# Kernel tuning notes

Hardware: AMD Instinct MI355X
Metric: run time of the kernel (lower is better)

The kernel has to match this reference:

```python
import jax, jax.numpy as jnp
import numpy as np
from jax import lax
from jax.scipy.special import logsumexp

NUM_TAGS = 17
INPUT_DIM = 1024
B, S = 256, 512


def setup_inputs() -> dict:
    key = jax.random.key(0)
    ks = jax.random.split(key, 7)
    data = jax.random.normal(ks[0], (B, S, INPUT_DIM), dtype=jnp.float32)
    labels = jax.random.randint(ks[1], (B, S), 0, NUM_TAGS)
    mask = jnp.ones((B, S), dtype=bool)  # torchcrf requires mask[:,0] all True
    W = jax.random.normal(ks[2], (NUM_TAGS, INPUT_DIM), dtype=jnp.float32) / np.sqrt(INPUT_DIM)
    b = jnp.zeros((NUM_TAGS,), dtype=jnp.float32)
    # torchcrf initializes transition params ~ U(-0.1, 0.1)
    start_trans = jax.random.uniform(ks[3], (NUM_TAGS,), minval=-0.1, maxval=0.1)
    end_trans = jax.random.uniform(ks[4], (NUM_TAGS,), minval=-0.1, maxval=0.1)
    transitions = jax.random.uniform(ks[5], (NUM_TAGS, NUM_TAGS), minval=-0.1, maxval=0.1)
    return {"data": data, "labels": labels, "mask": mask, "W": W, "b": b,
            "start_trans": start_trans, "end_trans": end_trans, "transitions": transitions}


def _crf_nll(data, labels, mask, W, b, start_trans, end_trans, transitions):
    # emissions: [B, S, T]
    em = jnp.einsum('bsd,td->bst', data, W) + b
    # time-major views
    em_t = em.transpose(1, 0, 2)          # [S, B, T]
    tags = labels.T                        # [S, B]
    m = mask.T.astype(em.dtype)            # [S, B]
    bidx = jnp.arange(data.shape[0])

    # ---- numerator: score of the gold path ----
    score0 = start_trans[tags[0]] + em_t[0, bidx, tags[0]]  # [B]

    def num_step(score, inp):
        e_t, tag_prev, tag_t, m_t = inp
        score = score + (transitions[tag_prev, tag_t] + e_t[bidx, tag_t]) * m_t
        return score, None

    score, _ = lax.scan(num_step, score0, (em_t[1:], tags[:-1], tags[1:], m[1:]))
    last_idx = mask.sum(axis=1).astype(jnp.int32) - 1
    last_tags = labels[bidx, last_idx]
    score = score + end_trans[last_tags]

    # ---- denominator: forward algorithm (log partition) ----
    alpha0 = start_trans[None, :] + em_t[0]  # [B, T]

    def den_step(alpha, inp):
        e_t, m_t = inp
        # [B, Tprev, Tnext]
        nxt = logsumexp(alpha[:, :, None] + transitions[None, :, :] + e_t[:, None, :], axis=1)
        alpha = jnp.where(m_t[:, None] > 0, nxt, alpha)
        return alpha, None

    alpha, _ = lax.scan(den_step, alpha0, (em_t[1:], m[1:]))
    denom = logsumexp(alpha + end_trans[None, :], axis=1)  # [B]

    llh = score - denom
    return -llh.mean()  # reduction='mean', module returns -loglik


def reference(data, labels, mask, W, b, start_trans, end_trans, transitions):
    return _crf_nll(data, labels, mask, W, b, start_trans, end_trans, transitions)
```

## Files before the change

### kernel.cpp

```cpp
#include <hip/hip_runtime.h>
#include <hip/hip_bf16.h>


#define BB 256
#define SS 512
#define DD 1024
#define TT 17
#define ROWS (BB * SS)

typedef float f32x4 __attribute__((ext_vector_type(4)));
typedef short s16x8 __attribute__((ext_vector_type(8)));

__device__ inline unsigned bfr(unsigned u) { return (u + 0x7fffu + ((u >> 16) & 1u)) >> 16; }
__device__ inline unsigned pk2(float x, float y) {
    return bfr(__float_as_uint(x)) | (bfr(__float_as_uint(y)) << 16);
}

__device__ inline void lds_barrier() {
    __builtin_amdgcn_s_waitcnt(0xC00F);
    __builtin_amdgcn_s_barrier();
}

__device__ inline float bcast(float x, int l) {
    return __uint_as_float((unsigned)__builtin_amdgcn_readlane((int)__float_as_uint(x), l));
}

#define LDA 40

__global__ __launch_bounds__(256) void emis_kernel(
    const float* __restrict__ data, const float* __restrict__ W,
    const float* __restrict__ bias, float* __restrict__ em)
{
    __shared__ __align__(16) short At[256 * LDA];
    const int tid = threadIdx.x;
    const size_t row0 = (size_t)blockIdx.x * 256;
    const int wv = tid >> 6, ln = tid & 63;
    const int nl = ln & 15, quad = ln >> 4;
    const int c4 = tid & 7, rr = tid >> 3;
    const bool w1act = (nl == 0);

    const float* gbase  = data + (row0 + rr) * DD + c4 * 4;
    const float* w0base = W + nl * DD + quad * 8;
    const float* w1base = W + 16 * DD + quad * 8;

    float4 a[8];
    float4 wa, wb, va, vb;
    va = make_float4(0.f, 0.f, 0.f, 0.f); vb = va;

#pragma unroll
    for (int i = 0; i < 8; i++) a[i] = *(const float4*)(gbase + (size_t)i * 32 * DD);
    wa = *(const float4*)(w0base);
    wb = *(const float4*)(w0base + 4);
    if (w1act) { va = *(const float4*)(w1base); vb = *(const float4*)(w1base + 4); }

    f32x4 acc[4][2];
#pragma unroll
    for (int m = 0; m < 4; m++) {
        acc[m][0] = (f32x4){0.f, 0.f, 0.f, 0.f};
        acc[m][1] = (f32x4){0.f, 0.f, 0.f, 0.f};
    }

    for (int ks = 0; ks < 32; ks++) {
        if (ks) lds_barrier();
#pragma unroll
        for (int i = 0; i < 8; i++) {
            uint2 p; p.x = pk2(a[i].x, a[i].y); p.y = pk2(a[i].z, a[i].w);
            *(uint2*)(&At[(rr + 32 * i) * LDA + c4 * 4]) = p;
        }
        union { s16x8 v; unsigned u[4]; } b0u, b1u;
        b0u.u[0] = pk2(wa.x, wa.y); b0u.u[1] = pk2(wa.z, wa.w);
        b0u.u[2] = pk2(wb.x, wb.y); b0u.u[3] = pk2(wb.z, wb.w);
        b1u.u[0] = pk2(va.x, va.y); b1u.u[1] = pk2(va.z, va.w);
        b1u.u[2] = pk2(vb.x, vb.y); b1u.u[3] = pk2(vb.z, vb.w);
        if (ks < 31) {
            const float* gn = gbase + (ks + 1) * 32;
#pragma unroll
            for (int i = 0; i < 8; i++) a[i] = *(const float4*)(gn + (size_t)i * 32 * DD);
            const float* w0n = w0base + (ks + 1) * 32;
            wa = *(const float4*)(w0n); wb = *(const float4*)(w0n + 4);
            if (w1act) {
                const float* w1n = w1base + (ks + 1) * 32;
                va = *(const float4*)(w1n); vb = *(const float4*)(w1n + 4);
            }
        }
        lds_barrier();
#pragma unroll
        for (int mt = 0; mt < 4; mt++) {
            s16x8 af = *(s16x8*)(&At[(wv * 64 + mt * 16 + nl) * LDA + quad * 8]);
            acc[mt][0] = __builtin_amdgcn_mfma_f32_16x16x32_bf16(af, b0u.v, acc[mt][0], 0, 0, 0);
            acc[mt][1] = __builtin_amdgcn_mfma_f32_16x16x32_bf16(af, b1u.v, acc[mt][1], 0, 0, 0);
        }
    }

    const float bs0 = bias[nl];
    const float bs16 = bias[16];
#pragma unroll
    for (int mt = 0; mt < 4; mt++) {
        const size_t rbase = row0 + wv * 64 + mt * 16 + quad * 4;
#pragma unroll
        for (int r = 0; r < 4; r++) {
            em[(rbase + r) * TT + nl] = acc[mt][0][r] + bs0;
            if (w1act) em[(rbase + r) * TT + 16] = acc[mt][1][r] + bs16;
        }
    }
}

__global__ __launch_bounds__(64) void crf_scan_kernel(
    const float* __restrict__ em, const int* __restrict__ labels,
    const float* __restrict__ start_t, const float* __restrict__ end_t,
    const float* __restrict__ trans, float* __restrict__ res)
{
    const int b = blockIdx.x;
    const int lane = threadIdx.x;
    const float* em_b = em + (size_t)b * SS * TT;
    const int* lab = labels + b * SS;
    __shared__ float sE[64 * TT + TT];

    float part = 0.f;
    for (int t = lane; t < SS; t += 64) {
        const int tag = lab[t];
        float c = em_b[t * TT + tag];
        if (t == 0) c += start_t[tag];
        else        c += trans[lab[t - 1] * TT + tag];
        if (t == SS - 1) c += end_t[tag];
        part += c;
    }
#pragma unroll
    for (int off = 32; off; off >>= 1) part += __shfl_xor(part, off);
    const float score = part;

    const bool act = lane < TT;
    const int j = act ? lane : 0;
    float Tcol[TT];
#pragma unroll
    for (int i = 0; i < TT; i++) Tcol[i] = __expf(trans[i * TT + j]);

    float A = act ? __expf(start_t[j] + em_b[j]) : 0.f;
    float logZ = 0.f;

    for (int t0 = 0; t0 < SS; t0 += 64) {
        __syncthreads();
#pragma unroll
        for (int i = 0; i < TT; i++) {
            const int flat = i * 64 + lane;
            sE[flat] = __expf(em_b[t0 * TT + flat]);
        }
        __syncthreads();
        int dt = (t0 == 0) ? 1 : 0;
        float e = sE[dt * TT + j];
        for (; dt < 64; dt++) {
            const float en = sE[(dt + 1) * TT + j];
            float v0 = bcast(A, 0) * Tcol[0];
            float v1 = bcast(A, 1) * Tcol[1];
            float v2 = bcast(A, 2) * Tcol[2];
            float v3 = bcast(A, 3) * Tcol[3];
#pragma unroll
            for (int i = 4; i < 16; i += 4) {
                v0 = fmaf(bcast(A, i + 0), Tcol[i + 0], v0);
                v1 = fmaf(bcast(A, i + 1), Tcol[i + 1], v1);
                v2 = fmaf(bcast(A, i + 2), Tcol[i + 2], v2);
                v3 = fmaf(bcast(A, i + 3), Tcol[i + 3], v3);
            }
            v0 = fmaf(bcast(A, 16), Tcol[16], v0);
            A = ((v0 + v1) + (v2 + v3)) * e;
            if (((t0 + dt) & 3) == 3) {
                const float s = bcast(A, 0);
                const float r = __builtin_amdgcn_rcpf(s);
                logZ -= __logf(r);
                A *= r;
            }
            e = en;
        }
    }

    float fv = act ? A * __expf(end_t[j]) : 0.f;
#pragma unroll
    for (int off = 16; off; off >>= 1) fv += __shfl_xor(fv, off);
    const float denom = logZ + __logf(fv);

    if (lane == 0) res[b] = denom - score;
}

__global__ __launch_bounds__(256) void reduce_kernel(
    const float* __restrict__ res, float* __restrict__ out)
{
    const int tid = threadIdx.x;
    float v = res[tid];
#pragma unroll
    for (int off = 32; off; off >>= 1) v += __shfl_xor(v, off);
    __shared__ float ws[4];
    if ((tid & 63) == 0) ws[tid >> 6] = v;
    __syncthreads();
    if (tid == 0) out[0] = (ws[0] + ws[1] + ws[2] + ws[3]) * (1.0f / BB);
}

extern "C" void kernel_launch(void* const* d_in, const int* in_sizes, int n_in,
                              void* d_out, int out_size, void* d_ws, size_t ws_size,
                              hipStream_t stream) {
    const float* data   = (const float*)d_in[0];
    const int*   labels = (const int*)d_in[1];
    const float* W      = (const float*)d_in[3];
    const float* bias   = (const float*)d_in[4];
    const float* st     = (const float*)d_in[5];
    const float* en     = (const float*)d_in[6];
    const float* trans  = (const float*)d_in[7];

    float* em  = (float*)d_ws;
    float* res = (float*)((char*)d_ws + (size_t)ROWS * TT * 4);

    emis_kernel<<<ROWS / 256, 256, 0, stream>>>(data, W, bias, em);
    crf_scan_kernel<<<BB, 64, 0, stream>>>(em, labels, st, en, trans, res);
    reduce_kernel<<<1, 256, 0, stream>>>(res, (float*)d_out);
}
```

Measured before the change: 792.5 us.

## Fuse emission GEMM and CRF scan into one producer-consumer kernel per batch row

Replaces the separate emission GEMM kernel and CRF scan kernel with a single kernel per batch element. Four waves compute 64-timestep chunks of emissions with MFMA, with W held in bf16 in LDS. A fifth wave runs the forward recursion and the gold-path score on the previous chunk through double-buffered LDS. This removes the global round trip of the emission tensor and overlaps the serial scan with the streaming of `data`. The trade-off is only 256 blocks of 5 waves, so latency hiding for the large input read depends on register prefetching.

```diff
diff --git a/kernel.cpp b/kernel.cpp
--- a/kernel.cpp
+++ b/kernel.cpp
@@ -6,7 +6,6 @@
 #define SS 512
 #define DD 1024
 #define TT 17
-#define ROWS (BB * SS)
 
 typedef float f32x4 __attribute__((ext_vector_type(4)));
 typedef short s16x8 __attribute__((ext_vector_type(8)));
@@ -25,160 +24,157 @@
     return __uint_as_float((unsigned)__builtin_amdgcn_readlane((int)__float_as_uint(x), l));
 }
 
-#define LDA 40
-
-__global__ __launch_bounds__(256) void emis_kernel(
-    const float* __restrict__ data, const float* __restrict__ W,
-    const float* __restrict__ bias, float* __restrict__ em)
-{
-    __shared__ __align__(16) short At[256 * LDA];
-    const int tid = threadIdx.x;
-    const size_t row0 = (size_t)blockIdx.x * 256;
-    const int wv = tid >> 6, ln = tid & 63;
-    const int nl = ln & 15, quad = ln >> 4;
-    const int c4 = tid & 7, rr = tid >> 3;
-    const bool w1act = (nl == 0);
-
-    const float* gbase  = data + (row0 + rr) * DD + c4 * 4;
-    const float* w0base = W + nl * DD + quad * 8;
-    const float* w1base = W + 16 * DD + quad * 8;
-
-    float4 a[8];
-    float4 wa, wb, va, vb;
-    va = make_float4(0.f, 0.f, 0.f, 0.f); vb = va;
-
-#pragma unroll
-    for (int i = 0; i < 8; i++) a[i] = *(const float4*)(gbase + (size_t)i * 32 * DD);
-    wa = *(const float4*)(w0base);
-    wb = *(const float4*)(w0base + 4);
-    if (w1act) { va = *(const float4*)(w1base); vb = *(const float4*)(w1base + 4); }
-
-    f32x4 acc[4][2];
-#pragma unroll
-    for (int m = 0; m < 4; m++) {
-        acc[m][0] = (f32x4){0.f, 0.f, 0.f, 0.f};
-        acc[m][1] = (f32x4){0.f, 0.f, 0.f, 0.f};
-    }
-
-    for (int ks = 0; ks < 32; ks++) {
-        if (ks) lds_barrier();
-#pragma unroll
-        for (int i = 0; i < 8; i++) {
-            uint2 p; p.x = pk2(a[i].x, a[i].y); p.y = pk2(a[i].z, a[i].w);
-            *(uint2*)(&At[(rr + 32 * i) * LDA + c4 * 4]) = p;
-        }
-        union { s16x8 v; unsigned u[4]; } b0u, b1u;
-        b0u.u[0] = pk2(wa.x, wa.y); b0u.u[1] = pk2(wa.z, wa.w);
-        b0u.u[2] = pk2(wb.x, wb.y); b0u.u[3] = pk2(wb.z, wb.w);
-        b1u.u[0] = pk2(va.x, va.y); b1u.u[1] = pk2(va.z, va.w);
-        b1u.u[2] = pk2(vb.x, vb.y); b1u.u[3] = pk2(vb.z, vb.w);
-        if (ks < 31) {
-            const float* gn = gbase + (ks + 1) * 32;
-#pragma unroll
-            for (int i = 0; i < 8; i++) a[i] = *(const float4*)(gn + (size_t)i * 32 * DD);
-            const float* w0n = w0base + (ks + 1) * 32;
-            wa = *(const float4*)(w0n); wb = *(const float4*)(w0n + 4);
-            if (w1act) {
-                const float* w1n = w1base + (ks + 1) * 32;
-                va = *(const float4*)(w1n); vb = *(const float4*)(w1n + 4);
-            }
-        }
-        lds_barrier();
-#pragma unroll
-        for (int mt = 0; mt < 4; mt++) {
-            s16x8 af = *(s16x8*)(&At[(wv * 64 + mt * 16 + nl) * LDA + quad * 8]);
-            acc[mt][0] = __builtin_amdgcn_mfma_f32_16x16x32_bf16(af, b0u.v, acc[mt][0], 0, 0, 0);
-            acc[mt][1] = __builtin_amdgcn_mfma_f32_16x16x32_bf16(af, b1u.v, acc[mt][1], 0, 0, 0);
-        }
-    }
-
-    const float bs0 = bias[nl];
-    const float bs16 = bias[16];
-#pragma unroll
-    for (int mt = 0; mt < 4; mt++) {
-        const size_t rbase = row0 + wv * 64 + mt * 16 + quad * 4;
-#pragma unroll
-        for (int r = 0; r < 4; r++) {
-            em[(rbase + r) * TT + nl] = acc[mt][0][r] + bs0;
-            if (w1act) em[(rbase + r) * TT + 16] = acc[mt][1][r] + bs16;
-        }
-    }
-}
-
-__global__ __launch_bounds__(64) void crf_scan_kernel(
-    const float* __restrict__ em, const int* __restrict__ labels,
+#define WLD 1032
+#define EROW (64 * TT)
+#define ESZ  (EROW + 32)
+
+__global__ __launch_bounds__(320) void crf_fused_kernel(
+    const float* __restrict__ data, const int* __restrict__ labels,
+    const float* __restrict__ W, const float* __restrict__ bias,
     const float* __restrict__ start_t, const float* __restrict__ end_t,
     const float* __restrict__ trans, float* __restrict__ res)
 {
+    __shared__ __align__(16) short Wl[18 * WLD];
+    __shared__ float sEe[2][ESZ];
+    __shared__ float sEr[2][ESZ];
+    __shared__ float sTr[TT * TT];
+
+    const int tid = threadIdx.x;
     const int b = blockIdx.x;
-    const int lane = threadIdx.x;
-    const float* em_b = em + (size_t)b * SS * TT;
-    const int* lab = labels + b * SS;
-    __shared__ float sE[64 * TT + TT];
-
-    float part = 0.f;
-    for (int t = lane; t < SS; t += 64) {
-        const int tag = lab[t];
-        float c = em_b[t * TT + tag];
-        if (t == 0) c += start_t[tag];
-        else        c += trans[lab[t - 1] * TT + tag];
-        if (t == SS - 1) c += end_t[tag];
-        part += c;
-    }
-#pragma unroll
-    for (int off = 32; off; off >>= 1) part += __shfl_xor(part, off);
-    const float score = part;
-
+    const int wv = tid >> 6, ln = tid & 63;
+    const int nl = ln & 15, quad = ln >> 4;
+
+    const float* rbase = data + ((size_t)b * SS + wv * 16 + nl) * DD + quad * 8;
+    float4 pa[4], pb[4];
+    if (wv < 4) {
+#pragma unroll
+        for (int k = 0; k < 4; k++) {
+            pa[k] = *(const float4*)(rbase + k * 32);
+            pb[k] = *(const float4*)(rbase + k * 32 + 4);
+        }
+    }
+
+    for (int i = tid; i < (TT * DD) / 4; i += 320) {
+        const int row = i >> 8;
+        const int col = (i & 255) * 4;
+        float4 w4 = *(const float4*)(W + row * DD + col);
+        uint2 p; p.x = pk2(w4.x, w4.y); p.y = pk2(w4.z, w4.w);
+        *(uint2*)(&Wl[row * WLD + col]) = p;
+    }
+    if (tid < 256) {
+        uint2 z; z.x = 0u; z.y = 0u;
+        *(uint2*)(&Wl[17 * WLD + tid * 4]) = z;
+    }
+    if (tid < TT * TT) sTr[tid] = trans[tid];
+    __syncthreads();
+
+    const short* w0p = &Wl[nl * WLD + quad * 8];
+    const short* w1p = &Wl[(nl == 0 ? 16 : 17) * WLD + quad * 8];
+    const float bs0 = bias[nl];
+    const float bs16 = bias[16];
+
+    const int lane = ln;
     const bool act = lane < TT;
     const int j = act ? lane : 0;
+    const int* lab = labels + b * SS;
     float Tcol[TT];
-#pragma unroll
-    for (int i = 0; i < TT; i++) Tcol[i] = __expf(trans[i * TT + j]);
-
-    float A = act ? __expf(start_t[j] + em_b[j]) : 0.f;
-    float logZ = 0.f;
-
-    for (int t0 = 0; t0 < SS; t0 += 64) {
-        __syncthreads();
-#pragma unroll
-        for (int i = 0; i < TT; i++) {
-            const int flat = i * 64 + lane;
-            sE[flat] = __expf(em_b[t0 * TT + flat]);
+    float A = 0.f, logZ = 0.f, numer = 0.f;
+    if (wv == 4) {
+#pragma unroll
+        for (int i = 0; i < TT; i++) Tcol[i] = __expf(sTr[i * TT + j]);
+    }
+
+    for (int it = 0; it < 9; ++it) {
+        if (wv < 4 && it < 8) {
+            const int bi = it & 1;
+            const float* rb = rbase + (size_t)it * 64 * DD;
+            const float* rbn = rb + 64 * DD;
+            f32x4 acc0 = {0.f, 0.f, 0.f, 0.f};
+            f32x4 acc1 = {0.f, 0.f, 0.f, 0.f};
+#pragma unroll
+            for (int ks = 0; ks < 32; ks++) {
+                const float4 ca = pa[ks & 3], cb = pb[ks & 3];
+                const float* pf = (ks < 28) ? (rb + (ks + 4) * 32)
+                                : (it < 7) ? (rbn + (ks - 28) * 32)
+                                           : rb;
+                pa[ks & 3] = *(const float4*)(pf);
+                pb[ks & 3] = *(const float4*)(pf + 4);
+                union { s16x8 v; unsigned u[4]; } af;
+                af.u[0] = pk2(ca.x, ca.y); af.u[1] = pk2(ca.z, ca.w);
+                af.u[2] = pk2(cb.x, cb.y); af.u[3] = pk2(cb.z, cb.w);
+                s16x8 b0 = *(const s16x8*)(w0p + ks * 32);
+                s16x8 b1 = *(const s16x8*)(w1p + ks * 32);
+                acc0 = __builtin_amdgcn_mfma_f32_16x16x32_bf16(af.v, b0, acc0, 0, 0, 0);
+                acc1 = __builtin_amdgcn_mfma_f32_16x16x32_bf16(af.v, b1, acc1, 0, 0, 0);
+            }
+#pragma unroll
+            for (int r = 0; r < 4; r++) {
+                const int dt = wv * 16 + quad * 4 + r;
+                const float raw = acc0[r] + bs0;
+                sEr[bi][dt * TT + nl] = raw;
+                sEe[bi][dt * TT + nl] = __expf(raw);
+                if (nl == 0) {
+                    const float r16 = acc1[r] + bs16;
+                    sEr[bi][dt * TT + 16] = r16;
+                    sEe[bi][dt * TT + 16] = __expf(r16);
+                }
+            }
         }
-        __syncthreads();
-        int dt = (t0 == 0) ? 1 : 0;
-        float e = sE[dt * TT + j];
-        for (; dt < 64; dt++) {
-            const float en = sE[(dt + 1) * TT + j];
-            float v0 = bcast(A, 0) * Tcol[0];
-            float v1 = bcast(A, 1) * Tcol[1];
-            float v2 = bcast(A, 2) * Tcol[2];
-            float v3 = bcast(A, 3) * Tcol[3];
-#pragma unroll
-            for (int i = 4; i < 16; i += 4) {
-                v0 = fmaf(bcast(A, i + 0), Tcol[i + 0], v0);
-                v1 = fmaf(bcast(A, i + 1), Tcol[i + 1], v1);
-                v2 = fmaf(bcast(A, i + 2), Tcol[i + 2], v2);
-                v3 = fmaf(bcast(A, i + 3), Tcol[i + 3], v3);
-            }
-            v0 = fmaf(bcast(A, 16), Tcol[16], v0);
-            A = ((v0 + v1) + (v2 + v3)) * e;
-            if (((t0 + dt) & 3) == 3) {
-                const float s = bcast(A, 0);
-                const float r = __builtin_amdgcn_rcpf(s);
-                logZ -= __logf(r);
-                A *= r;
-            }
-            e = en;
+        if (wv == 4 && it >= 1) {
+            const int t = it - 1;
+            const int bi = t & 1;
+            {
+                const int tg = t * 64 + lane;
+                const int tag = lab[tg];
+                float c = sEr[bi][lane * TT + tag];
+                if (tg == 0) c += start_t[tag];
+                else         c += sTr[lab[tg - 1] * TT + tag];
+                if (tg == SS - 1) c += end_t[tag];
+                numer += c;
+            }
+            int dt = 0;
+            if (t == 0) {
+                A = act ? __expf(start_t[j] + sEr[0][j]) : 0.f;
+                dt = 1;
+            }
+            float e = sEe[bi][dt * TT + j];
+            for (; dt < 64; dt++) {
+                const float en = sEe[bi][(dt + 1) * TT + j];
+                float v0 = bcast(A, 0) * Tcol[0];
+                float v1 = bcast(A, 1) * Tcol[1];
+                float v2 = bcast(A, 2) * Tcol[2];
+                float v3 = bcast(A, 3) * Tcol[3];
+#pragma unroll
+                for (int i = 4; i < 16; i += 4) {
+                    v0 = fmaf(bcast(A, i + 0), Tcol[i + 0], v0);
+                    v1 = fmaf(bcast(A, i + 1), Tcol[i + 1], v1);
+                    v2 = fmaf(bcast(A, i + 2), Tcol[i + 2], v2);
+                    v3 = fmaf(bcast(A, i + 3), Tcol[i + 3], v3);
+                }
+                v0 = fmaf(bcast(A, 16), Tcol[16], v0);
+                A = ((v0 + v1) + (v2 + v3)) * e;
+                if (((t * 64 + dt) & 3) == 3) {
+                    const float s = bcast(A, 0);
+                    const float rcp = __builtin_amdgcn_rcpf(s);
+                    logZ -= __logf(rcp);
+                    A *= rcp;
+                }
+                e = en;
+            }
         }
-    }
-
-    float fv = act ? A * __expf(end_t[j]) : 0.f;
-#pragma unroll
-    for (int off = 16; off; off >>= 1) fv += __shfl_xor(fv, off);
-    const float denom = logZ + __logf(fv);
-
-    if (lane == 0) res[b] = denom - score;
+        lds_barrier();
+    }
+
+    if (wv == 4) {
+        float part = numer;
+#pragma unroll
+        for (int off = 32; off; off >>= 1) part += __shfl_xor(part, off);
+        float fv = act ? A * __expf(end_t[j]) : 0.f;
+#pragma unroll
+        for (int off = 16; off; off >>= 1) fv += __shfl_xor(fv, off);
+        const float denom = logZ + __logf(fv);
+        if (lane == 0) res[b] = denom - part;
+    }
 }
 
 __global__ __launch_bounds__(256) void reduce_kernel(
@@ -205,10 +201,8 @@
     const float* en     = (const float*)d_in[6];
     const float* trans  = (const float*)d_in[7];
 
-    float* em  = (float*)d_ws;
-    float* res = (float*)((char*)d_ws + (size_t)ROWS * TT * 4);
-
-    emis_kernel<<<ROWS / 256, 256, 0, stream>>>(data, W, bias, em);
-    crf_scan_kernel<<<BB, 64, 0, stream>>>(em, labels, st, en, trans, res);
+    float* res = (float*)d_ws;
+
+    crf_fused_kernel<<<BB, 320, 0, stream>>>(data, labels, W, bias, st, en, trans, res);
     reduce_kernel<<<1, 256, 0, stream>>>(res, (float*)d_out);
 }
```

After: 706.0 us. 10.9% less time.
